# Kernel optimization log

Measured on AMD Instinct MI355X. Metric: run time of the kernel, lower is better.

## Reference

```python
import jax, jax.numpy as jnp
import numpy as np

V, D, C, L, F = 32000, 1024, 2048, 6, 4096
B, S = 2, 2048


def _layer_norm(x, w, b, eps=1e-5):
    mu = jnp.mean(x, axis=-1, keepdims=True)
    var = jnp.mean(jnp.square(x - mu), axis=-1, keepdims=True)
    return (x - mu) * jax.lax.rsqrt(var + eps) * w + b


def setup_inputs() -> dict:
    key = jax.random.key(0)
    ks = jax.random.split(key, 16)
    s = 0.02
    inp = {
        "tokens": jax.random.randint(ks[0], (B, S), 0, V),
        "embed_table": jax.random.normal(ks[1], (V, D), jnp.float32) * s,
        "pos_table": jax.random.normal(ks[2], (C, D), jnp.float32) * s,
        # stacked per-layer params [L, ...]
        "ln1_w": jnp.ones((L, D), jnp.float32),
        "ln1_b": jnp.zeros((L, D), jnp.float32),
        "qkv_w": jax.random.normal(ks[3], (L, 3 * D, D), jnp.float32) * s,
        "qkv_b": jnp.zeros((L, 3 * D), jnp.float32),
        "ln2_w": jnp.ones((L, D), jnp.float32),
        "ln2_b": jnp.zeros((L, D), jnp.float32),
        "ffa_w": jax.random.normal(ks[4], (L, F, D), jnp.float32) * s,
        "ffa_b": jnp.zeros((L, F), jnp.float32),
        "ffb_w": jax.random.normal(ks[5], (L, D, F), jnp.float32) * s,
        "ffb_b": jnp.zeros((L, D), jnp.float32),
        "out_w": jax.random.normal(ks[6], (V, D), jnp.float32) * s,
    }
    return inp


def _forward(tokens, embed_table, pos_table, ln1_w, ln1_b, qkv_w, qkv_b,
             ln2_w, ln2_b, ffa_w, ffa_b, ffb_w, ffb_b, out_w):
    Sx = tokens.shape[1]
    h = embed_table[tokens] + pos_table[:Sx][None, :, :]  # [B,S,D]
    causal = jnp.triu(jnp.ones((Sx, Sx), bool), k=1)       # True = masked
    scale = jnp.float32(D) ** 0.5

    def block(h, p):
        l1w, l1b, qw, qb, l2w, l2b, aw, ab, bw, bb = p
        a = _layer_norm(h, l1w, l1b)
        qkv = jnp.einsum('bsd,ed->bse', a, qw) + qb       # [B,S,3D]
        q, k, v = jnp.split(qkv, 3, axis=-1)
        scores = jnp.einsum('bsd,btd->bst', q, k)          # [B,S,S]
        scores = jnp.where(causal[None], -jnp.inf, scores)
        attn = jax.nn.softmax(scores / scale, axis=-1)
        h = h + jnp.einsum('bst,btd->bsd', attn, v)
        f = _layer_norm(h, l2w, l2b)
        f = jax.nn.relu(jnp.einsum('bsd,fd->bsf', f, aw) + ab)
        h = h + jnp.einsum('bsf,df->bsd', f, bw) + bb
        return h, None

    params = (ln1_w, ln1_b, qkv_w, qkv_b, ln2_w, ln2_b, ffa_w, ffa_b, ffb_w, ffb_b)
    h, _ = jax.lax.scan(block, h, params)
    # OutputLayer applies only the Linear (output_norm is defined but unused)
    return jnp.einsum('bsd,vd->bsv', h, out_w)


def reference(tokens, embed_table, pos_table, ln1_w, ln1_b, qkv_w, qkv_b,
              ln2_w, ln2_b, ffa_w, ffa_b, ffb_w, ffb_b, out_w):
    return _forward(tokens, embed_table, pos_table, ln1_w, ln1_b, qkv_w, qkv_b,
                    ln2_w, ln2_b, ffa_w, ffa_b, ffb_w, ffb_b, out_w)
```

## Files before the change

### kernel.cpp

```cpp
#include <hip/hip_runtime.h>

#define Dm 1024
#define Sm 2048
#define Bm 2
#define Lm 6
#define Fm 4096
#define Vm 32000
#define MT (Bm*Sm)

typedef unsigned short u16;
typedef unsigned int   u32;
typedef __attribute__((ext_vector_type(8))) short bf16x8;
typedef __attribute__((ext_vector_type(4))) float f32x4;

__device__ __forceinline__ u16 f2bf(float f) {
  u32 u = __float_as_uint(f);
  u += 0x7fffu + ((u >> 16) & 1u);
  return (u16)(u >> 16);
}
__device__ __forceinline__ u32 pack2(float a, float b) {
  return (u32)f2bf(a) | ((u32)f2bf(b) << 16);
}
__device__ __forceinline__ void gload16(const void* g, void* l) {
  __builtin_amdgcn_global_load_lds(
      (const __attribute__((address_space(1))) void*)g,
      (__attribute__((address_space(3))) void*)l, 16, 0, 0);
}

__global__ __launch_bounds__(256) void embed_kernel(
    const int* __restrict__ tok, const float* __restrict__ emb,
    const float* __restrict__ pos, float* __restrict__ h)
{
  int i  = blockIdx.x * 256 + threadIdx.x;
  int d  = (i & (Dm/4 - 1)) * 4;
  int bs = i >> 8;
  int s  = bs & (Sm - 1);
  int t  = tok[bs];
  float4 e = *(const float4*)(emb + (size_t)t * Dm + d);
  float4 p = *(const float4*)(pos + (size_t)s * Dm + d);
  float4 r; r.x = e.x + p.x; r.y = e.y + p.y; r.z = e.z + p.z; r.w = e.w + p.w;
  *(float4*)(h + (size_t)bs * Dm + d) = r;
}

__global__ __launch_bounds__(256) void ln_kernel(
    const float* __restrict__ x, const float* __restrict__ w,
    const float* __restrict__ b, u16* __restrict__ o)
{
  __shared__ float red[8];
  int row = blockIdx.x, tid = threadIdx.x;
  const float* xr = x + (size_t)row * Dm;
  float4 v = *(const float4*)(xr + tid * 4);
  float s1 = v.x + v.y + v.z + v.w;
  float s2 = v.x*v.x + v.y*v.y + v.z*v.z + v.w*v.w;
  #pragma unroll
  for (int off = 32; off; off >>= 1) {
    s1 += __shfl_down(s1, off, 64);
    s2 += __shfl_down(s2, off, 64);
  }
  int lane = tid & 63, wv = tid >> 6;
  if (!lane) { red[wv] = s1; red[4 + wv] = s2; }
  __syncthreads();
  s1 = red[0] + red[1] + red[2] + red[3];
  s2 = red[4] + red[5] + red[6] + red[7];
  float mu = s1 * (1.f / Dm);
  float rs = rsqrtf(s2 * (1.f / Dm) - mu * mu + 1e-5f);
  float4 wv4 = *(const float4*)(w + tid * 4);
  float4 bv4 = *(const float4*)(b + tid * 4);
  uint2 pk;
  pk.x = pack2((v.x - mu) * rs * wv4.x + bv4.x, (v.y - mu) * rs * wv4.y + bv4.y);
  pk.y = pack2((v.z - mu) * rs * wv4.z + bv4.z, (v.w - mu) * rs * wv4.w + bv4.w);
  *(uint2*)(o + (size_t)row * Dm + tid * 4) = pk;
}

__global__ __launch_bounds__(256) void softmax_kernel(
    const float* __restrict__ sc, u16* __restrict__ at)
{
  __shared__ float red[8];
  int gr = blockIdx.x;
  int s  = gr & (Sm - 1);
  const float* x = sc + (size_t)gr * Sm;
  u16* o = at + (size_t)gr * Sm;
  int tid = threadIdx.x;
  float4 v0 = *(const float4*)(x + tid * 8);
  float4 v1 = *(const float4*)(x + tid * 8 + 4);
  float vals[8] = {v0.x, v0.y, v0.z, v0.w, v1.x, v1.y, v1.z, v1.w};
  float mx = -1e30f;
  #pragma unroll
  for (int j = 0; j < 8; ++j) {
    int t = tid * 8 + j;
    vals[j] = (t <= s) ? vals[j] * 0.03125f : -1e30f;
    mx = fmaxf(mx, vals[j]);
  }
  #pragma unroll
  for (int off = 32; off; off >>= 1) mx = fmaxf(mx, __shfl_down(mx, off, 64));
  int lane = tid & 63, wv = tid >> 6;
  if (!lane) red[wv] = mx;
  __syncthreads();
  mx = fmaxf(fmaxf(red[0], red[1]), fmaxf(red[2], red[3]));
  __syncthreads();
  float e[8], sm = 0.f;
  #pragma unroll
  for (int j = 0; j < 8; ++j) {
    int t = tid * 8 + j;
    e[j] = (t <= s) ? __expf(vals[j] - mx) : 0.f;
    sm += e[j];
  }
  #pragma unroll
  for (int off = 32; off; off >>= 1) sm += __shfl_down(sm, off, 64);
  if (!lane) red[wv] = sm;
  __syncthreads();
  sm = red[0] + red[1] + red[2] + red[3];
  float inv = 1.f / sm;
  uint4 p;
  p.x = pack2(e[0]*inv, e[1]*inv); p.y = pack2(e[2]*inv, e[3]*inv);
  p.z = pack2(e[4]*inv, e[5]*inv); p.w = pack2(e[6]*inv, e[7]*inv);
  *(uint4*)(o + tid * 8) = p;
}

__global__ __launch_bounds__(256) void cvt8_kernel(
    const float* __restrict__ x, u16* __restrict__ o)
{
  size_t i = ((size_t)blockIdx.x * 256 + threadIdx.x) * 8;
  float4 v0 = *(const float4*)(x + i);
  float4 v1 = *(const float4*)(x + i + 4);
  uint4 p; p.x = pack2(v0.x, v0.y); p.y = pack2(v0.z, v0.w);
  p.z = pack2(v1.x, v1.y); p.w = pack2(v1.z, v1.w);
  *(uint4*)(o + i) = p;
}

__global__ __launch_bounds__(256) void cvtw_kernel(
    const float* __restrict__ qw, const float* __restrict__ aw,
    const float* __restrict__ bw, u16* __restrict__ o)
{
  int b = blockIdx.x;
  const float* src; u16* dst; int idx;
  if (b < 1536)      { src = qw; dst = o;                     idx = b; }
  else if (b < 3584) { src = aw; dst = o + 3*Dm*Dm;           idx = b - 1536; }
  else               { src = bw; dst = o + 3*Dm*Dm + Fm*Dm;   idx = b - 3584; }
  size_t i = ((size_t)idx * 256 + threadIdx.x) * 8;
  float4 v0 = *(const float4*)(src + i);
  float4 v1 = *(const float4*)(src + i + 4);
  uint4 p; p.x = pack2(v0.x, v0.y); p.y = pack2(v0.z, v0.w);
  p.z = pack2(v1.x, v1.y); p.w = pack2(v1.z, v1.w);
  *(uint4*)(dst + i) = p;
}

__global__ __launch_bounds__(256) void vtr_kernel(
    const u16* __restrict__ v, u16* __restrict__ vT)
{
  __shared__ u16 t[64][64];
  int b = blockIdx.z;
  int s0 = blockIdx.x * 64, d0 = blockIdx.y * 64;
  const u16* src = v + ((size_t)b * Sm + s0) * (3 * Dm) + d0;
  int tid = threadIdx.x;
  int rr = tid >> 3, cc = (tid & 7) * 8;
  #pragma unroll
  for (int it = 0; it < 2; ++it) {
    int r = rr + it * 32;
    uint4 x = *(const uint4*)(src + (size_t)r * (3 * Dm) + cc);
    *(uint4*)&t[r][cc ^ (((r >> 3) & 7) << 3)] = x;
  }
  __syncthreads();
  u16* dst = vT + ((size_t)b * Dm + d0) * Sm + s0;
  #pragma unroll
  for (int it = 0; it < 2; ++it) {
    int d = rr + it * 32;
    u16 tmp[8];
    #pragma unroll
    for (int j = 0; j < 8; ++j) {
      int r = cc + j;
      tmp[j] = t[r][d ^ (((r >> 3) & 7) << 3)];
    }
    *(uint4*)(dst + (size_t)d * Sm + cc) = *(uint4*)tmp;
  }
}

enum { EPI_F32 = 0, EPI_BF16 = 1, EPI_RELU_BF16 = 2, EPI_RES = 3, EPI_F32NT = 4 };

__global__ __launch_bounds__(256, 2)
void gemm_kernel(const u16* __restrict__ A, const u16* __restrict__ B,
                 float* __restrict__ outF, u16* __restrict__ outB,
                 const float* __restrict__ bias, const float* __restrict__ resid,
                 int N, int K, int lda, int ldb,
                 long sA, long sB, long sO, long sR,
                 int mshift, int epi, int swz, int cmode)
{
  __shared__ __align__(16) short As[2][128 * 64];
  __shared__ __align__(16) short Bs[2][128 * 64];

  const int z = blockIdx.z;
  int bid = blockIdx.x;
  if (swz) { int cpx = gridDim.x >> 3; bid = (bid & 7) * cpx + (bid >> 3); }
  const int m0 = (bid & ((1 << mshift) - 1)) << 7;
  const int n0 = (bid >> mshift) << 7;

  if (cmode == 1 && n0 > m0) return;
  const int keff = (cmode == 2) ? min(K, m0 + 128) : K;
  const int nt = keff >> 6;

  const u16* Az = A + (size_t)z * sA;
  const u16* Bz = B + (size_t)z * sB;

  const int tid = threadIdx.x;
  const int l   = tid & 63;
  const int w   = tid >> 6;
  const int sub = l >> 3;
  const int colb = ((l & 7) ^ sub) << 4;
  const int row0 = w * 32 + sub;

  const char* gA = (const char*)(Az + (size_t)(m0 + row0) * lda) + colb;
  const char* gB = (const char*)(Bz + (size_t)(n0 + row0) * ldb) + colb;
  const size_t stepA = (size_t)8 * lda * 2;
  const size_t stepB = (size_t)8 * ldb * 2;

  const int wm   = (w >> 1) * 64;
  const int wn   = (w & 1) * 64;
  const int lrow = l & 15;
  const int kgrp = l >> 4;

  f32x4 acc[4][4];
  #pragma unroll
  for (int i = 0; i < 4; ++i)
    #pragma unroll
    for (int j = 0; j < 4; ++j)
      acc[i][j] = (f32x4){0.f, 0.f, 0.f, 0.f};

  auto STAGE = [&](int buf, int t) {
    const char* ga = gA + (size_t)t * 128;
    const char* gb = gB + (size_t)t * 128;
    char* la = (char*)As[buf] + w * 4096;
    char* lb = (char*)Bs[buf] + w * 4096;
    #pragma unroll
    for (int c = 0; c < 4; ++c) {
      gload16(ga + c * stepA, la + c * 1024);
      gload16(gb + c * stepB, lb + c * 1024);
    }
  };

  STAGE(0, 0);
  __syncthreads();

  for (int t = 0; t < nt; ++t) {
    const int cur = t & 1;
    if (t + 1 < nt) STAGE(cur ^ 1, t + 1);
    const char* bA = (const char*)As[cur];
    const char* bB = (const char*)Bs[cur];
    #pragma unroll
    for (int kk = 0; kk < 2; ++kk) {
      bf16x8 af[4], bf_[4];
      #pragma unroll
      for (int i = 0; i < 4; ++i) {
        int ar = wm + i * 16 + lrow;
        af[i]  = *(const bf16x8*)(bA + ar * 128 +
                                  ((kk * 64 + kgrp * 16) ^ ((ar & 7) << 4)));
        int br = wn + i * 16 + lrow;
        bf_[i] = *(const bf16x8*)(bB + br * 128 +
                                  ((kk * 64 + kgrp * 16) ^ ((br & 7) << 4)));
      }
      #pragma unroll
      for (int i = 0; i < 4; ++i)
        #pragma unroll
        for (int j = 0; j < 4; ++j)
          acc[i][j] = __builtin_amdgcn_mfma_f32_16x16x32_bf16(af[i], bf_[j], acc[i][j], 0, 0, 0);
    }
    __syncthreads();
  }

  #pragma unroll
  for (int i = 0; i < 4; ++i) {
    #pragma unroll
    for (int j = 0; j < 4; ++j) {
      #pragma unroll
      for (int r = 0; r < 4; ++r) {
        int m = m0 + wm + i * 16 + kgrp * 4 + r;
        int n = n0 + wn + j * 16 + lrow;
        float v = acc[i][j][r];
        if (bias) v += bias[n];
        if (epi == EPI_F32) {
          outF[(size_t)z * sO + (size_t)m * N + n] = v;
        } else if (epi == EPI_F32NT) {
          __builtin_nontemporal_store(v, outF + (size_t)m * N + n);
        } else if (epi == EPI_BF16) {
          outB[(size_t)m * N + n] = f2bf(v);
        } else if (epi == EPI_RELU_BF16) {
          outB[(size_t)m * N + n] = f2bf(fmaxf(v, 0.f));
        } else {
          float* o = outF + (size_t)z * sO;
          const float* rsd = resid + (size_t)z * sR;
          o[(size_t)m * N + n] = rsd[(size_t)m * N + n] + v;
        }
      }
    }
  }
}

extern "C" void kernel_launch(void* const* d_in, const int* in_sizes, int n_in,
                              void* d_out, int out_size, void* d_ws, size_t ws_size,
                              hipStream_t stream)
{
  const int*   tok  = (const int*)d_in[0];
  const float* emb  = (const float*)d_in[1];
  const float* pos  = (const float*)d_in[2];
  const float* ln1w = (const float*)d_in[3];
  const float* ln1b = (const float*)d_in[4];
  const float* qkvw = (const float*)d_in[5];
  const float* qkvb = (const float*)d_in[6];
  const float* ln2w = (const float*)d_in[7];
  const float* ln2b = (const float*)d_in[8];
  const float* ffaw = (const float*)d_in[9];
  const float* ffab = (const float*)d_in[10];
  const float* ffbw = (const float*)d_in[11];
  const float* ffbb = (const float*)d_in[12];
  const float* outw = (const float*)d_in[13];
  float* out = (float*)d_out;

  char* p = (char*)d_ws;
  float* h      = (float*)p;  p += (size_t)MT * Dm * 4;
  u16*   a      = (u16*)p;    p += (size_t)MT * Dm * 2;
  u16*   hb     = (u16*)p;    p += (size_t)MT * Dm * 2;
  u16*   qkv    = (u16*)p;    p += (size_t)MT * 3 * Dm * 2;
  u16*   vT     = (u16*)p;    p += (size_t)Bm * Dm * Sm * 2;
  float* scores = (float*)p;  p += (size_t)Bm * Sm * Sm * 4;
  u16*   attn   = (u16*)p;    p += (size_t)Bm * Sm * Sm * 2;
  u16*   f      = (u16*)p;    p += (size_t)MT * Fm * 2;
  u16*   wlb    = (u16*)p;    p += (size_t)(3*Dm*Dm + Fm*Dm + Dm*Fm) * 2;
  u16*   owb    = qkv;

  embed_kernel<<<MT * Dm / 1024, 256, 0, stream>>>(tok, emb, pos, h);

  for (int l = 0; l < Lm; ++l) {
    cvtw_kernel<<<5632, 256, 0, stream>>>(
        qkvw + (size_t)l * 3 * Dm * Dm, ffaw + (size_t)l * Fm * Dm,
        ffbw + (size_t)l * Dm * Fm, wlb);
    ln_kernel<<<MT, 256, 0, stream>>>(h, ln1w + l * Dm, ln1b + l * Dm, a);
    gemm_kernel<<<dim3(768, 1, 1), 256, 0, stream>>>(
        a, wlb, nullptr, qkv, qkvb + l * 3 * Dm, nullptr,
        3 * Dm, Dm, Dm, Dm, 0, 0, 0, 0, 5, EPI_BF16, 1, 0);
    gemm_kernel<<<dim3(256, 1, Bm), 256, 0, stream>>>(
        qkv, qkv + Dm, scores, nullptr, nullptr, nullptr,
        Sm, Dm, 3 * Dm, 3 * Dm, (long)Sm * 3 * Dm, (long)Sm * 3 * Dm,
        (long)Sm * Sm, 0, 4, EPI_F32, 0, 1);
    softmax_kernel<<<Bm * Sm, 256, 0, stream>>>(scores, attn);
    vtr_kernel<<<dim3(32, 16, Bm), 256, 0, stream>>>(qkv + 2 * Dm, vT);
    gemm_kernel<<<dim3(128, 1, Bm), 256, 0, stream>>>(
        attn, vT, h, nullptr, nullptr, h,
        Dm, Sm, Sm, Sm, (long)Sm * Sm, (long)Dm * Sm,
        (long)Sm * Dm, (long)Sm * Dm, 4, EPI_RES, 0, 2);
    ln_kernel<<<MT, 256, 0, stream>>>(h, ln2w + l * Dm, ln2b + l * Dm, a);
    gemm_kernel<<<dim3(1024, 1, 1), 256, 0, stream>>>(
        a, wlb + 3 * Dm * Dm, nullptr, f, ffab + l * Fm, nullptr,
        Fm, Dm, Dm, Dm, 0, 0, 0, 0, 5, EPI_RELU_BF16, 1, 0);
    gemm_kernel<<<dim3(256, 1, 1), 256, 0, stream>>>(
        f, wlb + 3 * Dm * Dm + Fm * Dm, h, nullptr, ffbb + l * Dm, h,
        Dm, Fm, Fm, Fm, 0, 0, 0, 0, 5, EPI_RES, 1, 0);
  }

  cvt8_kernel<<<MT * Dm / 2048, 256, 0, stream>>>(h, hb);
  cvt8_kernel<<<Vm * Dm / 2048, 256, 0, stream>>>(outw, owb);
  gemm_kernel<<<dim3(8000, 1, 1), 256, 0, stream>>>(
      hb, owb, out, nullptr, nullptr, nullptr,
      Vm, Dm, Dm, Dm, 0, 0, 0, 0, 5, EPI_F32NT, 1, 0);
}
```

Measured before the change: 2.480 ms.

## Load B fragments directly from global into registers, single-buffer A in LDS

The GEMM kernel stops staging the B tile through shared memory. Each wave now reads its B MFMA fragments straight from global memory into registers, and only A is staged into one LDS buffer with a barrier before and after the load. This cuts LDS use and LDS traffic for B and could raise occupancy. In exchange it drops the double-buffered overlap of loads with compute, and the B global reads are strided and partly duplicated across waves, which risks exposed latency.

```diff
diff --git a/kernel.cpp b/kernel.cpp
--- a/kernel.cpp
+++ b/kernel.cpp
@@ -185,8 +185,7 @@
                  long sA, long sB, long sO, long sR,
                  int mshift, int epi, int swz, int cmode)
 {
-  __shared__ __align__(16) short As[2][128 * 64];
-  __shared__ __align__(16) short Bs[2][128 * 64];
+  __shared__ __align__(16) short As[128 * 64];
 
   const int z = blockIdx.z;
   int bid = blockIdx.x;
@@ -196,7 +195,6 @@
 
   if (cmode == 1 && n0 > m0) return;
   const int keff = (cmode == 2) ? min(K, m0 + 128) : K;
-  const int nt = keff >> 6;
 
   const u16* Az = A + (size_t)z * sA;
   const u16* Bz = B + (size_t)z * sB;
@@ -209,15 +207,16 @@
   const int row0 = w * 32 + sub;
 
   const char* gA = (const char*)(Az + (size_t)(m0 + row0) * lda) + colb;
-  const char* gB = (const char*)(Bz + (size_t)(n0 + row0) * ldb) + colb;
   const size_t stepA = (size_t)8 * lda * 2;
-  const size_t stepB = (size_t)8 * ldb * 2;
+  char* lA = (char*)As + w * 4096;
 
   const int wm   = (w >> 1) * 64;
   const int wn   = (w & 1) * 64;
   const int lrow = l & 15;
   const int kgrp = l >> 4;
 
+  const u16* gBf = Bz + (size_t)(n0 + wn + lrow) * ldb + kgrp * 8;
+
   f32x4 acc[4][4];
   #pragma unroll
   for (int i = 0; i < 4; ++i)
@@ -225,45 +224,36 @@
     for (int j = 0; j < 4; ++j)
       acc[i][j] = (f32x4){0.f, 0.f, 0.f, 0.f};
 
-  auto STAGE = [&](int buf, int t) {
-    const char* ga = gA + (size_t)t * 128;
-    const char* gb = gB + (size_t)t * 128;
-    char* la = (char*)As[buf] + w * 4096;
-    char* lb = (char*)Bs[buf] + w * 4096;
-    #pragma unroll
-    for (int c = 0; c < 4; ++c) {
-      gload16(ga + c * stepA, la + c * 1024);
-      gload16(gb + c * stepB, lb + c * 1024);
-    }
-  };
-
-  STAGE(0, 0);
-  __syncthreads();
-
-  for (int t = 0; t < nt; ++t) {
-    const int cur = t & 1;
-    if (t + 1 < nt) STAGE(cur ^ 1, t + 1);
-    const char* bA = (const char*)As[cur];
-    const char* bB = (const char*)Bs[cur];
+  for (int k0 = 0; k0 < keff; k0 += 64) {
+    bf16x8 bf_[2][4];
+    #pragma unroll
+    for (int kk = 0; kk < 2; ++kk)
+      #pragma unroll
+      for (int j = 0; j < 4; ++j)
+        bf_[kk][j] = *(const bf16x8*)(gBf + (size_t)(j * 16) * ldb + k0 + kk * 32);
+
+    __syncthreads();
+    const char* ga = gA + (size_t)k0 * 2;
+    #pragma unroll
+    for (int c = 0; c < 4; ++c)
+      gload16(ga + c * stepA, lA + c * 1024);
+    __syncthreads();
+
     #pragma unroll
     for (int kk = 0; kk < 2; ++kk) {
-      bf16x8 af[4], bf_[4];
+      bf16x8 af[4];
       #pragma unroll
       for (int i = 0; i < 4; ++i) {
         int ar = wm + i * 16 + lrow;
-        af[i]  = *(const bf16x8*)(bA + ar * 128 +
+        af[i]  = *(const bf16x8*)((const char*)As + ar * 128 +
                                   ((kk * 64 + kgrp * 16) ^ ((ar & 7) << 4)));
-        int br = wn + i * 16 + lrow;
-        bf_[i] = *(const bf16x8*)(bB + br * 128 +
-                                  ((kk * 64 + kgrp * 16) ^ ((br & 7) << 4)));
       }
       #pragma unroll
       for (int i = 0; i < 4; ++i)
         #pragma unroll
         for (int j = 0; j < 4; ++j)
-          acc[i][j] = __builtin_amdgcn_mfma_f32_16x16x32_bf16(af[i], bf_[j], acc[i][j], 0, 0, 0);
+          acc[i][j] = __builtin_amdgcn_mfma_f32_16x16x32_bf16(af[i], bf_[kk][j], acc[i][j], 0, 0, 0);
     }
-    __syncthreads();
   }
 
   #pragma unroll
```

Measured after the change: 3.356 ms. 1.35x slower.
